# Kernel optimization log

Hardware: AMD Instinct MI355X
Metric: run time of the kernel (lower is better)

The kernel has to match this reference:

```python
import jax, jax.numpy as jnp
import numpy as np

EPS = 1e-5
K = 32          # nsample in PCT sample_and_group
S1, S2 = 512, 256


def _bn_relu(h, gamma, beta, axes):
    # BatchNorm1d in training mode: batch stats over (batch, length) per channel (last axis here)
    mu = jnp.mean(h, axes, keepdims=True)
    var = jnp.var(h, axes, keepdims=True)
    return jax.nn.relu((h - mu) * jax.lax.rsqrt(var + EPS) * gamma + beta)


def _index_points(points, idx):
    # points [B,N,C], idx [B,...] int -> [B,...,C]
    return jax.vmap(lambda p, i: p[i])(points, idx)


def _fps(xyz, npoint):
    # farthest point sampling; deterministic start at index 0. xyz [B,N,3] -> [B,npoint] int32
    B, N, _ = xyz.shape

    def body(carry, _):
        dmin, far = carry
        c = jnp.take_along_axis(xyz, far[:, None, None], axis=1)  # [B,1,3]
        dmin = jnp.minimum(dmin, jnp.sum((xyz - c) ** 2, -1))     # [B,N]
        return (dmin, jnp.argmax(dmin, -1).astype(jnp.int32)), far

    init = (jnp.full((B, N), 1e10, xyz.dtype), jnp.zeros((B,), jnp.int32))
    _, idxs = jax.lax.scan(body, init, None, length=npoint)
    return jnp.transpose(idxs)  # [B, npoint]


def _sg(features, xyz, s, w1, g1, b1, w2, g2, b2):
    # features [B,N,C], xyz [B,N,3] -> (new_xyz [B,s,3], out [B,s,out_ch])
    xyz_c = jax.lax.stop_gradient(xyz)
    fps_idx = _fps(xyz_c, s)                       # [B,s]
    new_xyz = _index_points(xyz, fps_idx)          # [B,s,3]
    new_pts = _index_points(features, fps_idx)     # [B,s,C]
    q = jax.lax.stop_gradient(new_xyz)
    # squared distances centers->all points, [B,s,N]
    d = (jnp.sum(q * q, -1)[:, :, None] + jnp.sum(xyz_c * xyz_c, -1)[:, None, :]
         - 2.0 * jnp.einsum('bsc,bnc->bsn', q, xyz_c))
    _, knn = jax.lax.top_k(-d, K)                  # [B,s,K] nearest neighbors
    grouped = _index_points(features, knn)         # [B,s,K,C]
    rel = grouped - new_pts[:, :, None, :]
    feat = jnp.concatenate([rel, jnp.broadcast_to(new_pts[:, :, None, :], rel.shape)], -1)  # [B,s,K,2C]
    h = _bn_relu(jnp.einsum('bskc,oc->bsko', feat, w1), g1, b1, (0, 1, 2))
    h = _bn_relu(jnp.einsum('bskc,oc->bsko', h, w2), g2, b2, (0, 1, 2))
    return new_xyz, jnp.max(h, axis=2)             # max over K neighbors -> [B,s,out]


def _forward(x, w1, g1, b1, w2, g2, b2,
             s1_w1, s1_g1, s1_b1, s1_w2, s1_g2, s1_b2,
             s2_w1, s2_g1, s2_b1, s2_w2, s2_g2, s2_b2):
    xyz = jnp.transpose(x, (0, 2, 1))                                # [B,N,3]
    f = _bn_relu(jnp.einsum('bcn,oc->bno', x, w1), g1, b1, (0, 1))   # [B,N,64]
    f = _bn_relu(jnp.einsum('bnc,oc->bno', f, w2), g2, b2, (0, 1))   # [B,N,64]
    xyz1, f1 = _sg(f, xyz, S1, s1_w1, s1_g1, s1_b1, s1_w2, s1_g2, s1_b2)   # [B,512,128]
    _, f2 = _sg(f1, xyz1, S2, s2_w1, s2_g1, s2_b1, s2_w2, s2_g2, s2_b2)    # [B,256,256]
    return jnp.transpose(f2, (0, 2, 1))                              # [B,256,256] channel-first


def setup_inputs() -> dict:
    key = jax.random.key(0)
    ks = jax.random.split(key, 8)
    B, N = 32, 4096
    inp = {"x": jax.random.normal(ks[0], (B, 3, N), jnp.float32)}

    def w(k, o, i):
        return jax.random.normal(k, (o, i), jnp.float32) * (1.0 / np.sqrt(i))

    inp["w1"] = w(ks[1], 64, 3);   inp["g1"] = jnp.ones((64,), jnp.float32);  inp["b1"] = jnp.zeros((64,), jnp.float32)
    inp["w2"] = w(ks[2], 64, 64);  inp["g2"] = jnp.ones((64,), jnp.float32);  inp["b2"] = jnp.zeros((64,), jnp.float32)
    inp["s1_w1"] = w(ks[3], 128, 128); inp["s1_g1"] = jnp.ones((128,), jnp.float32); inp["s1_b1"] = jnp.zeros((128,), jnp.float32)
    inp["s1_w2"] = w(ks[4], 128, 128); inp["s1_g2"] = jnp.ones((128,), jnp.float32); inp["s1_b2"] = jnp.zeros((128,), jnp.float32)
    inp["s2_w1"] = w(ks[5], 256, 256); inp["s2_g1"] = jnp.ones((256,), jnp.float32); inp["s2_b1"] = jnp.zeros((256,), jnp.float32)
    inp["s2_w2"] = w(ks[6], 256, 256); inp["s2_g2"] = jnp.ones((256,), jnp.float32); inp["s2_b2"] = jnp.zeros((256,), jnp.float32)
    return inp


def reference(x, w1, g1, b1, w2, g2, b2,
              s1_w1, s1_g1, s1_b1, s1_w2, s1_g2, s1_b2,
              s2_w1, s2_g1, s2_b1, s2_w2, s2_g2, s2_b2):
    return _forward(x, w1, g1, b1, w2, g2, b2,
                    s1_w1, s1_g1, s1_b1, s1_w2, s1_g2, s1_b2,
                    s2_w1, s2_g1, s2_b1, s2_w2, s2_g2, s2_b2)
```

## Files before the change

kernel.cpp:

```cpp
#include <hip/hip_runtime.h>

typedef short short8 __attribute__((ext_vector_type(8)));
typedef _Float16 h8 __attribute__((ext_vector_type(8)));
typedef float f32x4 __attribute__((ext_vector_type(4)));

#define DEVI __device__ __forceinline__

DEVI float h2f(short s) { return (float)__builtin_bit_cast(_Float16, s); }
DEVI short f2h(float f) { return __builtin_bit_cast(short, (_Float16)f); }
DEVI f32x4 mfma16(short8 a, short8 b, f32x4 c) {
  return __builtin_amdgcn_mfma_f32_16x16x32_f16(
      __builtin_bit_cast(h8, a), __builtin_bit_cast(h8, b), c, 0, 0, 0);
}

DEVI float wave_max_bcast(float v) {
  const int ID = 0xff800000;
  int x = __builtin_bit_cast(int, v);
#define STEPM(ctrl)                                                     \
  {                                                                     \
    int t = __builtin_amdgcn_update_dpp(ID, x, ctrl, 0xf, 0xf, false);  \
    x = __builtin_bit_cast(int, fmaxf(__builtin_bit_cast(float, x),     \
                                      __builtin_bit_cast(float, t)));   \
  }
  STEPM(0x111) STEPM(0x112) STEPM(0x114) STEPM(0x118) STEPM(0x142) STEPM(0x143)
#undef STEPM
  return __builtin_bit_cast(float, __builtin_amdgcn_readlane(x, 63));
}
DEVI float wave_min_bcast_f(float v) {
  const int ID = 0x7f800000;
  int x = __builtin_bit_cast(int, v);
#define STEPN(ctrl)                                                     \
  {                                                                     \
    int t = __builtin_amdgcn_update_dpp(ID, x, ctrl, 0xf, 0xf, false);  \
    x = __builtin_bit_cast(int, fminf(__builtin_bit_cast(float, x),     \
                                      __builtin_bit_cast(float, t)));   \
  }
  STEPN(0x111) STEPN(0x112) STEPN(0x114) STEPN(0x118) STEPN(0x142) STEPN(0x143)
#undef STEPN
  return __builtin_bit_cast(float, __builtin_amdgcn_readlane(x, 63));
}
DEVI unsigned wave_min_bcast_u(unsigned v) {
  const int ID = (int)0xffffffff;
  int x = (int)v;
#define STEPU(ctrl)                                                     \
  {                                                                     \
    int t = __builtin_amdgcn_update_dpp(ID, x, ctrl, 0xf, 0xf, false);  \
    x = (int)((unsigned)x < (unsigned)t ? (unsigned)x : (unsigned)t);   \
  }
  STEPU(0x111) STEPU(0x112) STEPU(0x114) STEPU(0x118) STEPU(0x142) STEPU(0x143)
#undef STEPU
  return (unsigned)__builtin_amdgcn_readlane(x, 63);
}
DEVI unsigned wave_iscan_add(unsigned v) {
  int x = (int)v, t;
  t = __builtin_amdgcn_update_dpp(0, x, 0x111, 0xf, 0xf, false); x += t;
  t = __builtin_amdgcn_update_dpp(0, x, 0x112, 0xf, 0xf, false); x += t;
  t = __builtin_amdgcn_update_dpp(0, x, 0x114, 0xf, 0xf, false); x += t;
  t = __builtin_amdgcn_update_dpp(0, x, 0x118, 0xf, 0xf, false); x += t;
  t = __builtin_amdgcn_update_dpp(0, x, 0x142, 0xa, 0xf, false); x += t;
  t = __builtin_amdgcn_update_dpp(0, x, 0x143, 0xc, 0xf, false); x += t;
  return (unsigned)x;
}

__global__ __launch_bounds__(256) void prep_kernel(
    const float* __restrict__ w2, const float* __restrict__ s1w2,
    const float* __restrict__ s2w2, const float* __restrict__ s1w1,
    const float* __restrict__ s2w1, short* __restrict__ w2b,
    short* __restrict__ s1w2b, short* __restrict__ s2w2b,
    short* __restrict__ W1pp, short* __restrict__ W2pp) {
  int i = blockIdx.x * 256 + threadIdx.x;
  if (i < 4096) {
    w2b[i] = f2h(w2[i]);
  } else if (i < 20480) {
    int j = i - 4096; s1w2b[j] = f2h(s1w2[j]);
  } else if (i < 86016) {
    int j = i - 20480; s2w2b[j] = f2h(s2w2[j]);
  } else if (i < 102400) {
    int j = i - 86016; int c = j & 127;
    float v = s1w1[j]; if (c >= 64) v -= s1w1[j - 64];
    W1pp[j] = f2h(v);
  } else if (i < 167936) {
    int j = i - 102400; int c = j & 255;
    float v = s2w1[j]; if (c >= 128) v -= s2w1[j - 128];
    W2pp[j] = f2h(v);
  }
}

__global__ __launch_bounds__(256) void stageA_kernel(
    const float* __restrict__ x, const float* __restrict__ w1,
    float* __restrict__ xyz, short* __restrict__ h0) {
  int i = blockIdx.x * 256 + threadIdx.x;
  int b = i >> 12, n = i & 4095;
  const float* xb = x + ((size_t)b * 3 << 12) + n;
  float x0 = xb[0], x1 = xb[4096], x2 = xb[8192];
  float* xp = xyz + (size_t)i * 3;
  xp[0] = x0; xp[1] = x1; xp[2] = x2;
  short* hp = h0 + ((size_t)i << 6);
#pragma unroll
  for (int o8 = 0; o8 < 8; ++o8) {
    short8 t;
#pragma unroll
    for (int j = 0; j < 8; ++j) {
      int o = o8 * 8 + j;
      float h = x0 * w1[o * 3] + x1 * w1[o * 3 + 1] + x2 * w1[o * 3 + 2];
      t[j] = f2h(h);
    }
    *reinterpret_cast<short8*>(hp + o8 * 8) = t;
  }
}


DEVI void stats64_body(int bid, int nb, int tid, const short* __restrict__ h,
                       float* __restrict__ partials, int M) {
  __shared__ float l0[256], l1[256];
  const int c = tid & 63, g = tid >> 6;
  float s0 = 0.f, s1 = 0.f;
  for (int m = bid * 4 + g; m < M; m += nb * 4) {
    float v = h2f(h[(size_t)m * 64 + c]);
    s0 += v; s1 += v * v;
  }
  l0[tid] = s0; l1[tid] = s1;
  __syncthreads();
  if (g == 0) {
    for (int w = 1; w < 4; ++w) { s0 += l0[c + w * 64]; s1 += l1[c + w * 64]; }
    partials[(size_t)c * nb + bid] = s0;
    partials[(size_t)(64 + c) * nb + bid] = s1;
  }
}

DEVI void reduce2_body(int c, int tid, const float* __restrict__ partials,
                       const float* __restrict__ gamma, const float* __restrict__ beta,
                       float* __restrict__ scale, float* __restrict__ shift,
                       int NB, int C, float invM) {
  __shared__ float l0[4], l1[4];
  const float* p0 = partials + (size_t)c * NB;
  const float* p1 = partials + (size_t)(C + c) * NB;
  float s0 = 0.f, s1 = 0.f;
  for (int i = tid; i < NB; i += 256) { s0 += p0[i]; s1 += p1[i]; }
#pragma unroll
  for (int off = 1; off < 64; off <<= 1) {
    s0 += __shfl_xor(s0, off);
    s1 += __shfl_xor(s1, off);
  }
  if ((tid & 63) == 0) { l0[tid >> 6] = s0; l1[tid >> 6] = s1; }
  __syncthreads();
  if (tid == 0) {
    s0 = l0[0] + l0[1] + l0[2] + l0[3];
    s1 = l1[0] + l1[1] + l1[2] + l1[3];
    float mean = s0 * invM;
    float var = fmaxf(s1 * invM - mean * mean, 0.f);
    float sc = gamma[c] / sqrtf(var + 1e-5f);
    scale[c] = sc;
    shift[c] = beta[c] - mean * sc;
  }
}

__global__ __launch_bounds__(256) void reduce2_kernel(
    const float* __restrict__ partials, const float* __restrict__ gamma,
    const float* __restrict__ beta, float* __restrict__ scale,
    float* __restrict__ shift, int NB, int C, float invM) {
  reduce2_body(blockIdx.x, threadIdx.x, partials, gamma, beta, scale, shift, NB, C, invM);
}

DEVI void apply_body(int bid, int tid, const short* __restrict__ h,
                     short* __restrict__ f, const float* __restrict__ scale,
                     const float* __restrict__ shift) {
  size_t i = ((size_t)bid * 256 + tid) * 8;
  int c0 = (int)(i & 63);
  short8 v = *reinterpret_cast<const short8*>(h + i);
  short8 o;
#pragma unroll
  for (int j = 0; j < 8; ++j) {
    float y = h2f(v[j]) * scale[c0 + j] + shift[c0 + j];
    o[j] = f2h(fmaxf(y, 0.f));
  }
  *reinterpret_cast<short8*>(f + i) = o;
}

template <int NPTS, int T>
DEVI void fps_seg_body(char* smemraw, int bid, int tid, const float* __restrict__ xyz,
                       int* __restrict__ out, float* __restrict__ xyzc, int nsel,
                       int it0, int it1, float* __restrict__ dming,
                       int* __restrict__ farg) {
  __builtin_amdgcn_s_setprio(1);
  constexpr int PT = NPTS / T;
  constexpr int NW = T / 64;
  float* sx = (float*)smemraw;
  float* sy = sx + NPTS;
  float* sz = sy + NPTS;
  float* wv = sz + NPTS;
  unsigned* wi = (unsigned*)(wv + 2 * NW);
  const int lane = tid & 63, wave = tid >> 6;
  const float* base = xyz + (size_t)bid * NPTS * 3;
  float px[PT], py[PT], pz[PT], dmin[PT];
#pragma unroll
  for (int j = 0; j < PT; ++j) {
    int n = j * T + tid;
    px[j] = base[n * 3]; py[j] = base[n * 3 + 1]; pz[j] = base[n * 3 + 2];
    sx[n] = px[j]; sy[n] = py[j]; sz[n] = pz[j];
  }
  int far;
  if (it0 == 0) {
#pragma unroll
    for (int j = 0; j < PT; ++j) dmin[j] = 1e10f;
    far = 0;
  } else {
#pragma unroll
    for (int j = 0; j < PT; ++j) dmin[j] = dming[(size_t)bid * NPTS + j * T + tid];
    far = farg[bid];
  }
  __syncthreads();
  float cx = sx[far], cy = sy[far], cz = sz[far];
  for (int it = it0; it < it1; ++it) {
    if (tid == 0) {
      out[bid * nsel + it] = far;
      if (xyzc) {
        float* xc = xyzc + ((size_t)bid * nsel + it) * 3;
        xc[0] = cx; xc[1] = cy; xc[2] = cz;
      }
    }
    float bv = -1.f;
#pragma unroll
    for (int j = 0; j < PT; ++j) {
      float dx = __fsub_rn(px[j], cx), dy = __fsub_rn(py[j], cy), dz = __fsub_rn(pz[j], cz);
      float d = __fadd_rn(__fadd_rn(__fmul_rn(dx, dx), __fmul_rn(dy, dy)), __fmul_rn(dz, dz));
      float dm = fminf(dmin[j], d);
      dmin[j] = dm;
      bv = fmaxf(bv, dm);
    }
    float wmv = wave_max_bcast(bv);
    unsigned ci = 0xffffffffu;
#pragma unroll
    for (int j = PT - 1; j >= 0; --j)
      if (dmin[j] == wmv) ci = (unsigned)(j * T + tid);
    unsigned wmi = wave_min_bcast_u(ci);
    const int bsel = it & 1;
    if (lane == 0) { wv[bsel * NW + wave] = wmv; wi[bsel * NW + wave] = wmi; }
    __syncthreads();
    const int e = lane & (NW - 1);
    float v = wv[bsel * NW + e];
    unsigned si = wi[bsel * NW + e];
#define CMB(ctrl)                                                                        \
  {                                                                                      \
    float v2 = __builtin_bit_cast(                                                       \
        float, __builtin_amdgcn_update_dpp(0, __builtin_bit_cast(int, v), ctrl, 0xf, 0xf, true)); \
    unsigned i2 = (unsigned)__builtin_amdgcn_update_dpp(0, (int)si, ctrl, 0xf, 0xf, true);\
    bool bt = (v2 > v) || (v2 == v && i2 < si);                                          \
    v = bt ? v2 : v; si = bt ? i2 : si;                                                  \
  }
    if constexpr (NW >= 2) CMB(0x121)
    if constexpr (NW >= 4) CMB(0x122)
    if constexpr (NW >= 8) CMB(0x124)
#undef CMB
    far = (int)si;
    cx = sx[far]; cy = sy[far]; cz = sz[far];
  }
  if (it1 < nsel) {
#pragma unroll
    for (int j = 0; j < PT; ++j) dming[(size_t)bid * NPTS + j * T + tid] = dmin[j];
    if (tid == 0) farg[bid] = far;
  }
}

#define KNN_SMEM_BYTES ((4096 + 256 + 4 + 256 + 256) * 4)
template <int NPTS, int S>
DEVI void knn_body(char* smemraw, int bs, int tid, const float* __restrict__ pts,
                   const int* __restrict__ fpsidx, int* __restrict__ knn) {
  constexpr int PT = NPTS / 256;
  unsigned* hist = (unsigned*)smemraw;
  unsigned* csums = hist + 4096;
  unsigned* meta = csums + 256;
  float* bval = (float*)(meta + 4);
  unsigned* bidx = (unsigned*)(bval + 256);
  const int lane = tid & 63, wave = tid >> 6;
  const int b = bs / S;
  const int cidx = fpsidx[bs];
  const float* cp = pts + ((size_t)b * NPTS + cidx) * 3;
  const float qx = cp[0], qy = cp[1], qz = cp[2];
  const float qq = __fadd_rn(__fadd_rn(__fmul_rn(qx, qx), __fmul_rn(qy, qy)), __fmul_rn(qz, qz));
  const float* base = pts + (size_t)b * NPTS * 3;
  float d[PT]; unsigned u[PT];
#pragma unroll
  for (int j = 0; j < PT; ++j) {
    int n = j * 256 + tid;
    float x = base[n * 3], y = base[n * 3 + 1], z = base[n * 3 + 2];
    float pp = __fadd_rn(__fadd_rn(__fmul_rn(x, x), __fmul_rn(y, y)), __fmul_rn(z, z));
    float dot = __fadd_rn(__fadd_rn(__fmul_rn(qx, x), __fmul_rn(qy, y)), __fmul_rn(qz, z));
    d[j] = __fsub_rn(__fadd_rn(qq, pp), __fmul_rn(2.f, dot));
    unsigned bits = __builtin_bit_cast(unsigned, d[j]);
    unsigned m = (unsigned)((int)bits >> 31);
    u[j] = bits ^ (m | 0x80000000u);
  }
  {
    uint4 z4 = {0u, 0u, 0u, 0u};
    uint4* hq = (uint4*)hist;
    for (int i = tid; i < 1024; i += 256) hq[i] = z4;
    if (tid == 0) { meta[0] = 0; meta[3] = 0; }
  }
  __syncthreads();
#pragma unroll
  for (int j = 0; j < PT; ++j) atomicAdd(&hist[u[j] >> 20], 1u);
  __syncthreads();
  {
    const uint4* hq = (const uint4*)(hist + tid * 16);
    unsigned cs = 0;
#pragma unroll
    for (int q = 0; q < 4; ++q) {
      uint4 v = hq[q];
      cs += v.x + v.y + v.z + v.w;
    }
    csums[tid] = cs;
  }
  __syncthreads();
  if (wave == 0) {
    const int t4 = lane * 4;
    unsigned c0 = csums[t4], c1 = csums[t4 + 1], c2 = csums[t4 + 2], c3 = csums[t4 + 3];
    unsigned lt = c0 + c1 + c2 + c3;
    unsigned incl = wave_iscan_add(lt);
    unsigned excl = incl - lt;
    unsigned long long blt = __ballot(incl >= 32u);
    int L = __ffsll((long long)blt) - 1;
    if (lane == L) {
      unsigned cum = excl;
      int bucket = -1;
      unsigned cc[4] = {c0, c1, c2, c3};
#pragma unroll
      for (int q = 0; q < 4; ++q) {
        if (bucket < 0 && cum + cc[q] >= 32u) {
          int bbase = (t4 + q) * 16;
          for (int h = 0; h < 16; ++h) {
            unsigned hv = hist[bbase + h];
            if (cum + hv >= 32u) { bucket = bbase + h; break; }
            cum += hv;
          }
        } else if (bucket < 0) {
          cum += cc[q];
        }
      }
      meta[1] = (unsigned)bucket;
      meta[2] = cum;
    }
  }
  __syncthreads();
  const unsigned B = meta[1];
  const unsigned cb = meta[2];
  int* kout = knn + (size_t)bs * 32;
#pragma unroll
  for (int j = 0; j < PT; ++j) {
    unsigned bk = u[j] >> 20;
    if (bk < B) {
      unsigned p = atomicAdd(&meta[0], 1u);
      kout[p] = j * 256 + tid;
    } else if (bk == B) {
      unsigned p = atomicAdd(&meta[3], 1u);
      if (p < 256u) { bval[p] = d[j]; bidx[p] = (unsigned)(j * 256 + tid); }
    }
  }
  __syncthreads();
  const int m = 32 - (int)cb;
  if (wave == 0 && m > 0) {
    unsigned nb = meta[3]; if (nb > 256u) nb = 256u;
    float v0 = (lane < (int)nb) ? bval[lane] : 3.4e38f;
    unsigned i0 = (lane < (int)nb) ? bidx[lane] : 0xffffffffu;
    float v1 = (lane + 64 < (int)nb) ? bval[lane + 64] : 3.4e38f;
    unsigned i1 = (lane + 64 < (int)nb) ? bidx[lane + 64] : 0xffffffffu;
    float v2 = (lane + 128 < (int)nb) ? bval[lane + 128] : 3.4e38f;
    unsigned i2 = (lane + 128 < (int)nb) ? bidx[lane + 128] : 0xffffffffu;
    float v3 = (lane + 192 < (int)nb) ? bval[lane + 192] : 3.4e38f;
    unsigned i3 = (lane + 192 < (int)nb) ? bidx[lane + 192] : 0xffffffffu;
    for (int k = 0; k < m; ++k) {
      float lv = v0; unsigned li = i0;
      if (v1 < lv || (v1 == lv && i1 < li)) { lv = v1; li = i1; }
      if (v2 < lv || (v2 == lv && i2 < li)) { lv = v2; li = i2; }
      if (v3 < lv || (v3 == lv && i3 < li)) { lv = v3; li = i3; }
      float wmv = wave_min_bcast_f(lv);
      unsigned ci = (lv == wmv) ? li : 0xffffffffu;
      unsigned wmi = wave_min_bcast_u(ci);
      if (lane == 0) kout[cb + k] = (int)wmi;
      if (i0 == wmi) { v0 = 3.4e38f; i0 = 0xffffffffu; }
      if (i1 == wmi) { v1 = 3.4e38f; i1 = 0xffffffffu; }
      if (i2 == wmi) { v2 = 3.4e38f; i2 = 0xffffffffu; }
      if (i3 == wmi) { v3 = 3.4e38f; i3 = 0xffffffffu; }
    }
  }
}

template <int KD, int ND, bool GATHER, bool BNA, int NPTS, int S, int EPI>
DEVI void gemm_body(char* smemraw, int bid, int tid, int gemmBlocks,
                    const short* A, const int* KNNp, const int* FPSp,
                    const short* __restrict__ W, const float* __restrict__ bnscale,
                    const float* __restrict__ bnshift, short* Hout,
                    float* __restrict__ mmax, float* __restrict__ mmin,
                    float* __restrict__ partials) {
  constexpr int C = KD / 2;
  constexpr int NT = (ND > 128) ? 8 : ND / 16;
  constexpr int BR = (ND > 128) ? 64 : 128;
  constexpr int KC = (ND >= 256) ? 64 : KD;
  constexpr int LOG2KC = (KC == 64) ? 6 : 7;
  constexpr int NCH = KD / KC;
  constexpr int KTC = KC / 32;
  constexpr int LROW = KC + 8;
  constexpr int TROW = ND + 8;
  constexpr int LBB = ND * LROW * 2;
  constexpr int TBB = BR * TROW * 2;
  constexpr int LSOFF = (LBB > TBB) ? LBB : TBB;
  short* lb = (short*)smemraw;
  float* lstats = (float*)(smemraw + LSOFF);
  const int wave = tid >> 6, lane = tid & 63;
  const int rowOff = (ND > 128) ? (wave >> 1) * 32 : wave * 32;
  const int colOff = (ND > 128) ? (wave & 1) * 128 : 0;
  const int mBase = bid * BR + rowOff;
  for (int i = tid; i < 2 * ND; i += 256) lstats[i] = 0.f;

  const short* aptr[2][2];
#pragma unroll
  for (int rg = 0; rg < 2; ++rg) {
    int m = mBase + rg * 16 + (lane & 15);
    if constexpr (GATHER) {
      int idx = KNNp[m];
      int bb = m / (S * 32);
      int s = (m - bb * (S * 32)) >> 5;
      int fidx = FPSp[bb * S + s];
      aptr[rg][0] = A + ((size_t)bb * NPTS + idx) * C;
      aptr[rg][1] = A + ((size_t)bb * NPTS + fidx) * C;
    } else {
      aptr[rg][0] = A + (size_t)m * KD;
      aptr[rg][1] = A + (size_t)m * KD + C;
    }
  }
  const int koLane = (lane >> 4) * 8;
  f32x4 acc[2][NT];
#pragma unroll
  for (int rg = 0; rg < 2; ++rg)
#pragma unroll
    for (int nt = 0; nt < NT; ++nt) acc[rg][nt] = (f32x4){0.f, 0.f, 0.f, 0.f};

#pragma unroll
  for (int ch = 0; ch < NCH; ++ch) {
    __syncthreads();
    constexpr int SIT = (ND * KC) / 2048;
#pragma unroll
    for (int i = 0; i < SIT; ++i) {
      int e = i * 2048 + tid * 8;
      int n = e >> LOG2KC, kk = e & (KC - 1);
      short8 v = *reinterpret_cast<const short8*>(W + (size_t)n * KD + ch * KC + kk);
      *reinterpret_cast<short8*>(&lb[n * LROW + kk]) = v;
    }
    __syncthreads();
#pragma unroll
    for (int ktc = 0; ktc < KTC; ++ktc) {
      const int kt = ch * KTC + ktc;
      const int half = (kt * 32 >= C) ? 1 : 0;
      const int ko = kt * 32 + koLane;
      const int koh = ko - half * C;
      short8 afrag[2];
#pragma unroll
      for (int rg = 0; rg < 2; ++rg) {
        short8 a = *reinterpret_cast<const short8*>(aptr[rg][half] + koh);
        if constexpr (BNA) {
          const float* scp = bnscale + ko;
          const float* shp = bnshift + ko;
#pragma unroll
          for (int j = 0; j < 8; ++j) {
            float v = h2f(a[j]);
            v = fmaxf(v * scp[j] + shp[j], 0.f);
            a[j] = f2h(v);
          }
        }
        afrag[rg] = a;
      }
#pragma unroll
      for (int nt = 0; nt < NT; ++nt) {
        short8 bfr = *reinterpret_cast<const short8*>(
            &lb[(colOff + nt * 16 + (lane & 15)) * LROW + ktc * 32 + koLane]);
        acc[0][nt] = mfma16(afrag[0], bfr, acc[0][nt]);
        acc[1][nt] = mfma16(afrag[1], bfr, acc[1][nt]);
      }
    }
  }
  __syncthreads();

#pragma unroll
  for (int nt = 0; nt < NT; ++nt) {
    float s0 = 0.f, s1 = 0.f;
#pragma unroll
    for (int rg = 0; rg < 2; ++rg)
#pragma unroll
      for (int i = 0; i < 4; ++i) {
        float v = acc[rg][nt][i];
        s0 += v; s1 += v * v;
      }
    s0 += __shfl_xor(s0, 16); s0 += __shfl_xor(s0, 32);
    s1 += __shfl_xor(s1, 16); s1 += __shfl_xor(s1, 32);
    if (lane < 16) {
      atomicAdd(&lstats[colOff + nt * 16 + lane], s0);
      atomicAdd(&lstats[ND + colOff + nt * 16 + lane], s1);
    }
  }

  if constexpr (EPI == 0) {
#pragma unroll
    for (int rg = 0; rg < 2; ++rg)
#pragma unroll
      for (int nt = 0; nt < NT; ++nt)
#pragma unroll
        for (int i = 0; i < 4; ++i) {
          int r = rowOff + rg * 16 + (lane >> 4) * 4 + i;
          int n = colOff + nt * 16 + (lane & 15);
          lb[r * TROW + n] = f2h(acc[rg][nt][i]);
        }
    __syncthreads();
    constexpr int TPR = ND / 8;
    constexpr int RPI = 256 / TPR;
    const int r0 = tid / TPR, c0 = (tid % TPR) * 8;
#pragma unroll
    for (int it = 0; it < BR / RPI; ++it) {
      int r = it * RPI + r0;
      short8 v = *reinterpret_cast<const short8*>(&lb[r * TROW + c0]);
      *reinterpret_cast<short8*>(&Hout[(size_t)(bid * BR + r) * ND + c0]) = v;
    }
  } else {
    const int center = (bid * BR + rowOff) >> 5;
#pragma unroll
    for (int nt = 0; nt < NT; ++nt) {
      float mx = -3.4e38f, mn = 3.4e38f;
#pragma unroll
      for (int rg = 0; rg < 2; ++rg)
#pragma unroll
        for (int i = 0; i < 4; ++i) {
          float v = acc[rg][nt][i];
          mx = fmaxf(mx, v); mn = fminf(mn, v);
        }
      mx = fmaxf(mx, __shfl_xor(mx, 16)); mx = fmaxf(mx, __shfl_xor(mx, 32));
      mn = fminf(mn, __shfl_xor(mn, 16)); mn = fminf(mn, __shfl_xor(mn, 32));
      if (lane < 16) {
        mmax[(size_t)center * ND + colOff + nt * 16 + lane] = mx;
        mmin[(size_t)center * ND + colOff + nt * 16 + lane] = mn;
      }
    }
    __syncthreads();
  }
  for (int i = tid; i < 2 * ND; i += 256)
    partials[(size_t)i * gemmBlocks + bid] = lstats[i];
}


template <int FN, int FT>
__global__ __launch_bounds__(256, 1) void fps_stats_seg(
    int fpsBlocks, const float* fxyz, int* fout, float* fxyzc, int fnsel,
    int it0, int it1, float* dming, int* farg,
    const short* sh, float* sp, int sM, int snb) {
  extern __shared__ char smem[];
  if ((int)blockIdx.x < fpsBlocks)
    fps_seg_body<FN, FT>(smem, blockIdx.x, threadIdx.x, fxyz, fout, fxyzc, fnsel,
                         it0, it1, dming, farg);
  else
    stats64_body(blockIdx.x - fpsBlocks, snb, threadIdx.x, sh, sp, sM);
}

template <int FN, int FT, int KNPTS, int KS>
__global__ __launch_bounds__(256, 1) void fps_r2_knn_seg(
    int fpsBlocks, int compBlocks, const float* fxyz, int* fout, float* fxyzc,
    int fnsel, int it0, int it1, float* dming, int* farg,
    const float* partials, const float* gamma, const float* beta,
    float* scale, float* shift, int NB, int C, float invM,
    const float* kpts, const int* kfps, int* kout, int ks0) {
  extern __shared__ char smem[];
  const int bx = (int)blockIdx.x;
  if (bx < fpsBlocks) {
    fps_seg_body<FN, FT>(smem, bx, threadIdx.x, fxyz, fout, fxyzc, fnsel,
                         it0, it1, dming, farg);
  } else if (bx < fpsBlocks + compBlocks) {
    reduce2_body(bx - fpsBlocks, threadIdx.x, partials, gamma, beta, scale,
                 shift, NB, C, invM);
  } else {
    int kb = bx - fpsBlocks - compBlocks;
    int bs = (kb >> 7) * KS + ks0 + (kb & 127);
    knn_body<KNPTS, KS>(smem, bs, threadIdx.x, kpts, kfps, kout);
  }
}

template <int FN, int FT, int KD, int ND, bool BNA, int EPI, int KNPTS, int KS>
__global__ __launch_bounds__(256, 1) void fps_gemm_knn_seg(
    int fpsBlocks, int compBlocks, const float* fxyz, int* fout, float* fxyzc,
    int fnsel, int it0, int it1, float* dming, int* farg,
    const short* A, const short* W, const float* bnscale, const float* bnshift,
    short* Hout, float* partials,
    const float* kpts, const int* kfps, int* kout, int ks0) {
  extern __shared__ char smem[];
  const int bx = (int)blockIdx.x;
  if (bx < fpsBlocks) {
    fps_seg_body<FN, FT>(smem, bx, threadIdx.x, fxyz, fout, fxyzc, fnsel,
                         it0, it1, dming, farg);
  } else if (bx < fpsBlocks + compBlocks) {
    gemm_body<KD, ND, false, BNA, 1, 1, EPI>(smem, bx - fpsBlocks, threadIdx.x,
                                             compBlocks, A, nullptr, nullptr,
                                             W, bnscale, bnshift, Hout, nullptr,
                                             nullptr, partials);
  } else {
    int kb = bx - fpsBlocks - compBlocks;
    int bs = (kb >> 7) * KS + ks0 + (kb & 127);
    knn_body<KNPTS, KS>(smem, bs, threadIdx.x, kpts, kfps, kout);
  }
}

template <int F2N, int NPTS, int S>
__global__ __launch_bounds__(256, 4) void fps2_knn_apply_kernel(
    int f2Blocks, const float* f2xyz, int* f2out, int f2nsel, int it0, int it1,
    float* dming2, int* farg2,
    int knnBlocks, const float* kpts, const int* kfps, int* kout, int ks0,
    const short* ah, short* af, const float* ascale, const float* ashift) {
  __shared__ __align__(16) char smem[KNN_SMEM_BYTES];
  const int bx = (int)blockIdx.x;
  if (bx < f2Blocks) {
    fps_seg_body<F2N, 256>(smem, bx, threadIdx.x, f2xyz, f2out, nullptr, f2nsel,
                           it0, it1, dming2, farg2);
  } else if (bx < f2Blocks + knnBlocks) {
    int kb = bx - f2Blocks;
    int bs = (kb >> 7) * S + ks0 + (kb & 127);
    knn_body<NPTS, S>(smem, bs, threadIdx.x, kpts, kfps, kout);
  } else {
    apply_body(bx - f2Blocks - knnBlocks, threadIdx.x, ah, af, ascale, ashift);
  }
}

template <int F2N, int KD, int ND, int NPTS, int S>
__global__ __launch_bounds__(256, 4) void mega1_kernel(
    int f2Blocks, const float* f2xyz, int* f2out, int f2nsel, int it0, int it1,
    float* dming2, int* farg2,
    const short* A, const int* KNNp, const int* FPSp, const short* W,
    short* Hout, float* partials) {
  extern __shared__ char smem[];
  const int bx = (int)blockIdx.x;
  if (bx < f2Blocks) {
    fps_seg_body<F2N, 256>(smem, bx, threadIdx.x, f2xyz, f2out, nullptr, f2nsel,
                           it0, it1, dming2, farg2);
  } else {
    int gb = bx - f2Blocks;
    const int gB = (int)gridDim.x - f2Blocks;
    const int q = gB >> 3;
    gb = (gb & 7) * q + (gb >> 3);
    gemm_body<KD, ND, true, false, NPTS, S, 0>(smem, gb, threadIdx.x, gB, A, KNNp,
                                               FPSp, W, nullptr, nullptr, Hout,
                                               nullptr, nullptr, partials);
  }
}

template <int F2N, int KD, int ND>
__global__ __launch_bounds__(256, 4) void fps2_gemm_kernel(
    int f2Blocks, const float* f2xyz, int* f2out, int f2nsel, int it0, int it1,
    float* dming2, int* farg2,
    const short* A, const short* W, const float* bnscale, const float* bnshift,
    float* mmax, float* mmin, float* partials) {
  extern __shared__ char smem[];
  const int bx = (int)blockIdx.x;
  if (bx < f2Blocks) {
    fps_seg_body<F2N, 256>(smem, bx, threadIdx.x, f2xyz, f2out, nullptr, f2nsel,
                           it0, it1, dming2, farg2);
  } else {
    gemm_body<KD, ND, false, true, 1, 1, 1>(smem, bx - f2Blocks, threadIdx.x,
                                            (int)gridDim.x - f2Blocks, A, nullptr,
                                            nullptr, W, bnscale, bnshift, nullptr,
                                            mmax, mmin, partials);
  }
}

template <int KD, int ND, bool GATHER, bool BNA, int NPTS, int S, int EPI>
__global__ __launch_bounds__(256, 4) void gemm_kernel(
    const short* A, const int* KNNp, const int* FPSp, const short* W,
    const float* bnscale, const float* bnshift, short* Hout,
    float* mmax, float* mmin, float* partials) {
  extern __shared__ char smem[];
  int bid = (int)blockIdx.x;
  if constexpr (GATHER) {
    const int q = (int)gridDim.x >> 3;
    bid = (bid & 7) * q + (bid >> 3);
  }
  gemm_body<KD, ND, GATHER, BNA, NPTS, S, EPI>(smem, bid, threadIdx.x,
                                               gridDim.x, A, KNNp, FPSp, W, bnscale,
                                               bnshift, Hout, mmax, mmin, partials);
}

template <int NPTS, int S>
__global__ __launch_bounds__(256, 4) void maxpool_knn_kernel(
    int knnBlocks, const float* pts, const int* fpsidx, int* knn,
    const float* mmax, const float* mmin, const float* scale, const float* shift,
    short* f1) {
  __shared__ __align__(16) char smem[KNN_SMEM_BYTES];
  if ((int)blockIdx.x < knnBlocks) {
    knn_body<NPTS, S>(smem, blockIdx.x, threadIdx.x, pts, fpsidx, knn);
  } else {
    const int ctr = (blockIdx.x - knnBlocks) * 2 + (threadIdx.x >> 7);
    const int c = threadIdx.x & 127;
    const float sc = scale[c], sh = shift[c];
    float y = (sc >= 0.f) ? mmax[(size_t)ctr * 128 + c] : mmin[(size_t)ctr * 128 + c];
    f1[(size_t)ctr * 128 + c] = f2h(fmaxf(sc * y + sh, 0.f));
  }
}

__global__ __launch_bounds__(256) void maxpool_out_kernel(
    const float* __restrict__ mmax, const float* __restrict__ mmin,
    const float* __restrict__ scale, const float* __restrict__ shift,
    float* __restrict__ out) {
  const int bs = blockIdx.x, c = threadIdx.x;
  const int b = bs >> 8, s = bs & 255;
  const float sc = scale[c], sh = shift[c];
  float y = (sc >= 0.f) ? mmax[(size_t)bs * 256 + c] : mmin[(size_t)bs * 256 + c];
  out[((size_t)b << 16) + ((size_t)c << 8) + s] = fmaxf(sc * y + sh, 0.f);
}

extern "C" void kernel_launch(void* const* d_in, const int* in_sizes, int n_in,
                              void* d_out, int out_size, void* d_ws, size_t ws_size,
                              hipStream_t stream) {
  (void)in_sizes; (void)n_in; (void)out_size; (void)ws_size;
  const float* x    = (const float*)d_in[0];
  const float* w1   = (const float*)d_in[1];
  const float* g1   = (const float*)d_in[2];
  const float* b1   = (const float*)d_in[3];
  const float* w2   = (const float*)d_in[4];
  const float* g2   = (const float*)d_in[5];
  const float* b2   = (const float*)d_in[6];
  const float* s1w1 = (const float*)d_in[7];
  const float* s1g1 = (const float*)d_in[8];
  const float* s1b1 = (const float*)d_in[9];
  const float* s1w2 = (const float*)d_in[10];
  const float* s1g2 = (const float*)d_in[11];
  const float* s1b2 = (const float*)d_in[12];
  const float* s2w1 = (const float*)d_in[13];
  const float* s2g1 = (const float*)d_in[14];
  const float* s2b1 = (const float*)d_in[15];
  const float* s2w2 = (const float*)d_in[16];
  const float* s2g2 = (const float*)d_in[17];
  const float* s2b2 = (const float*)d_in[18];
  float* out = (float*)d_out;

  char* ws = (char*)d_ws;
  size_t off = 0;
  auto alloc = [&](size_t bytes) -> char* {
    size_t p = (off + 255) & ~(size_t)255;
    off = p + bytes;
    return ws + p;
  };

  float* xyz      = (float*)alloc(32ull * 4096 * 3 * 4);
  short* h0       = (short*)alloc(32ull * 4096 * 64 * 2);
  short* hb       = (short*)alloc(32ull * 4096 * 64 * 2);
  short* fb       = (short*)alloc(32ull * 4096 * 64 * 2);
  int*   fps1     = (int*)alloc(32ull * 512 * 4);
  float* xyzc1    = (float*)alloc(32ull * 512 * 3 * 4);
  int*   knn1     = (int*)alloc(32ull * 512 * 32 * 4);
  short* f1       = (short*)alloc(32ull * 512 * 128 * 2);
  int*   fps2     = (int*)alloc(32ull * 256 * 4);
  int*   knn2     = (int*)alloc(32ull * 256 * 32 * 4);
  float* dming    = (float*)alloc(32ull * 4096 * 4);
  int*   farg     = (int*)alloc(32 * 4);
  float* dming2   = (float*)alloc(32ull * 512 * 4);
  int*   farg2    = (int*)alloc(32 * 4);
  short* hbuf     = (short*)alloc(134217728ull);
  float* mm1max   = (float*)alloc(16384ull * 128 * 4);
  float* mm1min   = (float*)alloc(16384ull * 128 * 4);
  float* mm2max   = (float*)alloc(8192ull * 256 * 4);
  float* mm2min   = (float*)alloc(8192ull * 256 * 4);
  float* partials = (float*)alloc(2ull * 256 * 4096 * 4);
  float* scA  = (float*)alloc(64 * 4);  float* shA  = (float*)alloc(64 * 4);
  float* scBc = (float*)alloc(64 * 4);  float* shBc = (float*)alloc(64 * 4);
  float* sc1a = (float*)alloc(128 * 4); float* sh1a = (float*)alloc(128 * 4);
  float* sc1b = (float*)alloc(128 * 4); float* sh1b = (float*)alloc(128 * 4);
  float* sc2a = (float*)alloc(256 * 4); float* sh2a = (float*)alloc(256 * 4);
  float* sc2b = (float*)alloc(256 * 4); float* sh2b = (float*)alloc(256 * 4);
  short* w2b   = (short*)alloc(4096 * 2);
  short* s1w2b = (short*)alloc(16384 * 2);
  short* s2w2b = (short*)alloc(65536 * 2);
  short* W1pp  = (short*)alloc(16384 * 2);
  short* W2pp  = (short*)alloc(65536 * 2);

  prep_kernel<<<656, 256, 0, stream>>>(w2, s1w2, s2w2, s1w1, s2w1, w2b, s1w2b, s2w2b, W1pp, W2pp);
  stageA_kernel<<<512, 256, 0, stream>>>(x, w1, xyz, h0);

  fps_stats_seg<4096, 256><<<288, 256, 49216, stream>>>(
      32, xyz, fps1, xyzc1, 512, 0, 128, dming, farg, h0, partials, 131072, 256);
  fps_r2_knn_seg<4096, 256, 4096, 512><<<4192, 256, 49216, stream>>>(
      32, 64, xyz, fps1, xyzc1, 512, 128, 256, dming, farg,
      partials, g1, b1, scA, shA, 256, 64, 1.f / 131072.f,
      xyz, fps1, knn1, 0);
  fps_gemm_knn_seg<4096, 256, 64, 64, true, 0, 4096, 512><<<5152, 256, 49216, stream>>>(
      32, 1024, xyz, fps1, xyzc1, 512, 256, 384, dming, farg,
      h0, w2b, scA, shA, hb, partials,
      xyz, fps1, knn1, 128);
  fps_r2_knn_seg<4096, 256, 4096, 512><<<4192, 256, 49216, stream>>>(
      32, 64, xyz, fps1, xyzc1, 512, 384, 512, dming, farg,
      partials, g2, b2, scBc, shBc, 1024, 64, 1.f / 131072.f,
      xyz, fps1, knn1, 256);

  fps2_knn_apply_kernel<512, 4096, 512><<<8224, 256, 0, stream>>>(
      32, xyzc1, fps2, 256, 0, 86, dming2, farg2,
      4096, xyz, fps1, knn1, 384, hb, fb, scBc, shBc);

  mega1_kernel<512, 128, 128, 4096, 512><<<4128, 256, 35840, stream>>>(
      32, xyzc1, fps2, 256, 86, 171, dming2, farg2,
      fb, knn1, fps1, W1pp, hbuf, partials);
  reduce2_kernel<<<128, 256, 0, stream>>>(partials, s1g1, s1b1, sc1a, sh1a, 4096, 128, 1.f / 524288.f);

  fps2_gemm_kernel<512, 128, 128><<<4128, 256, 35840, stream>>>(
      32, xyzc1, fps2, 256, 171, 256, dming2, farg2,
      hbuf, s1w2b, sc1a, sh1a, mm1max, mm1min, partials);
  reduce2_kernel<<<128, 256, 0, stream>>>(partials, s1g2, s1b2, sc1b, sh1b, 4096, 128, 1.f / 524288.f);

  maxpool_knn_kernel<512, 256><<<16384, 256, 0, stream>>>(
      8192, xyzc1, fps2, knn2, mm1max, mm1min, sc1b, sh1b, f1);

  gemm_kernel<256, 256, true, false, 512, 256, 0><<<4096, 256, 38912, stream>>>(
      f1, knn2, fps2, W2pp, nullptr, nullptr, hbuf, nullptr, nullptr, partials);
  reduce2_kernel<<<256, 256, 0, stream>>>(partials, s2g1, s2b1, sc2a, sh2a, 4096, 256, 1.f / 262144.f);
  gemm_kernel<256, 256, false, true, 1, 1, 1><<<4096, 256, 38912, stream>>>(
      hbuf, nullptr, nullptr, s2w2b, sc2a, sh2a, nullptr, mm2max, mm2min, partials);
  reduce2_kernel<<<256, 256, 0, stream>>>(partials, s2g2, s2b2, sc2b, sh2b, 4096, 256, 1.f / 262144.f);
  maxpool_out_kernel<<<8192, 256, 0, stream>>>(mm2max, mm2min, sc2b, sh2b, out);
}
```

Before: 795.2 us.

## Fold BN-apply into stage-1 gather GEMM and overlap it with KNN blocks

Removes the standalone BN+ReLU apply pass that wrote a normalized copy of the stage-0 features. The stage-1 gather GEMM now reads the raw features and applies scale/shift on load, using a duplicated 128-wide scale/shift table for the concatenated rel/center channels. Most GEMM blocks are moved into the FPS2/KNN kernel so they co-run with the remaining KNN work, and the rest stay in mega1. This saves a full read/write pass over the feature buffer, but every gathered neighbor now repeats the affine work, and correctness depends on KNN rows for each GEMM block being finished before that block runs.

```diff
diff --git a/kernel.cpp b/kernel.cpp
--- a/kernel.cpp
+++ b/kernel.cpp
@@ -131,7 +131,7 @@
 DEVI void reduce2_body(int c, int tid, const float* __restrict__ partials,
                        const float* __restrict__ gamma, const float* __restrict__ beta,
                        float* __restrict__ scale, float* __restrict__ shift,
-                       int NB, int C, float invM) {
+                       int NB, int C, float invM, int dupC) {
   __shared__ float l0[4], l1[4];
   const float* p0 = partials + (size_t)c * NB;
   const float* p1 = partials + (size_t)(C + c) * NB;
@@ -150,8 +150,10 @@
     float mean = s0 * invM;
     float var = fmaxf(s1 * invM - mean * mean, 0.f);
     float sc = gamma[c] / sqrtf(var + 1e-5f);
+    float sh = beta[c] - mean * sc;
     scale[c] = sc;
-    shift[c] = beta[c] - mean * sc;
+    shift[c] = sh;
+    if (dupC) { scale[c + C] = sc; shift[c + C] = sh; }
   }
 }
 
@@ -159,22 +161,8 @@
     const float* __restrict__ partials, const float* __restrict__ gamma,
     const float* __restrict__ beta, float* __restrict__ scale,
     float* __restrict__ shift, int NB, int C, float invM) {
-  reduce2_body(blockIdx.x, threadIdx.x, partials, gamma, beta, scale, shift, NB, C, invM);
-}
-
-DEVI void apply_body(int bid, int tid, const short* __restrict__ h,
-                     short* __restrict__ f, const float* __restrict__ scale,
-                     const float* __restrict__ shift) {
-  size_t i = ((size_t)bid * 256 + tid) * 8;
-  int c0 = (int)(i & 63);
-  short8 v = *reinterpret_cast<const short8*>(h + i);
-  short8 o;
-#pragma unroll
-  for (int j = 0; j < 8; ++j) {
-    float y = h2f(v[j]) * scale[c0 + j] + shift[c0 + j];
-    o[j] = f2h(fmaxf(y, 0.f));
-  }
-  *reinterpret_cast<short8*>(f + i) = o;
+  reduce2_body(blockIdx.x, threadIdx.x, partials, gamma, beta, scale, shift, NB, C,
+               invM, 0);
 }
 
 template <int NPTS, int T>
@@ -563,7 +551,7 @@
     int fpsBlocks, int compBlocks, const float* fxyz, int* fout, float* fxyzc,
     int fnsel, int it0, int it1, float* dming, int* farg,
     const float* partials, const float* gamma, const float* beta,
-    float* scale, float* shift, int NB, int C, float invM,
+    float* scale, float* shift, int NB, int C, float invM, int dupC,
     const float* kpts, const int* kfps, int* kout, int ks0) {
   extern __shared__ char smem[];
   const int bx = (int)blockIdx.x;
@@ -572,7 +560,7 @@
                          it0, it1, dming, farg);
   } else if (bx < fpsBlocks + compBlocks) {
     reduce2_body(bx - fpsBlocks, threadIdx.x, partials, gamma, beta, scale,
-                 shift, NB, C, invM);
+                 shift, NB, C, invM, dupC);
   } else {
     int kb = bx - fpsBlocks - compBlocks;
     int bs = (kb >> 7) * KS + ks0 + (kb & 127);
@@ -604,32 +592,43 @@
   }
 }
 
-template <int F2N, int NPTS, int S>
-__global__ __launch_bounds__(256, 4) void fps2_knn_apply_kernel(
+template <int F2N, int KNPTS, int KS, int KD, int ND, int NPTS, int S,
+          int JCNT, int JOFF, int BPB>
+__global__ __launch_bounds__(256, 4) void fps2_knn_gemm_kernel(
     int f2Blocks, const float* f2xyz, int* f2out, int f2nsel, int it0, int it1,
     float* dming2, int* farg2,
     int knnBlocks, const float* kpts, const int* kfps, int* kout, int ks0,
-    const short* ah, short* af, const float* ascale, const float* ashift) {
-  __shared__ __align__(16) char smem[KNN_SMEM_BYTES];
+    const short* A, const int* KNNp, const int* FPSp, const short* W,
+    const float* bnscale, const float* bnshift, short* Hout, float* partials,
+    int gemmTotal) {
+  extern __shared__ char smem[];
   const int bx = (int)blockIdx.x;
   if (bx < f2Blocks) {
     fps_seg_body<F2N, 256>(smem, bx, threadIdx.x, f2xyz, f2out, nullptr, f2nsel,
                            it0, it1, dming2, farg2);
   } else if (bx < f2Blocks + knnBlocks) {
     int kb = bx - f2Blocks;
-    int bs = (kb >> 7) * S + ks0 + (kb & 127);
-    knn_body<NPTS, S>(smem, bs, threadIdx.x, kpts, kfps, kout);
+    int bs = (kb >> 7) * KS + ks0 + (kb & 127);
+    knn_body<KNPTS, KS>(smem, bs, threadIdx.x, kpts, kfps, kout);
   } else {
-    apply_body(bx - f2Blocks - knnBlocks, threadIdx.x, ah, af, ascale, ashift);
-  }
-}
-
-template <int F2N, int KD, int ND, int NPTS, int S>
+    int gb = bx - f2Blocks - knnBlocks;
+    const int gB = (int)gridDim.x - f2Blocks - knnBlocks;
+    const int q = gB >> 3;
+    gb = (gb & 7) * q + (gb >> 3);
+    int bid = (gb / JCNT) * BPB + JOFF + (gb % JCNT);
+    gemm_body<KD, ND, true, true, NPTS, S, 0>(smem, bid, threadIdx.x, gemmTotal,
+                                              A, KNNp, FPSp, W, bnscale, bnshift,
+                                              Hout, nullptr, nullptr, partials);
+  }
+}
+
+template <int F2N, int KD, int ND, int NPTS, int S, int JCNT, int JOFF, int BPB>
 __global__ __launch_bounds__(256, 4) void mega1_kernel(
     int f2Blocks, const float* f2xyz, int* f2out, int f2nsel, int it0, int it1,
     float* dming2, int* farg2,
     const short* A, const int* KNNp, const int* FPSp, const short* W,
-    short* Hout, float* partials) {
+    const float* bnscale, const float* bnshift, short* Hout, float* partials,
+    int gemmTotal) {
   extern __shared__ char smem[];
   const int bx = (int)blockIdx.x;
   if (bx < f2Blocks) {
@@ -640,9 +639,11 @@
     const int gB = (int)gridDim.x - f2Blocks;
     const int q = gB >> 3;
     gb = (gb & 7) * q + (gb >> 3);
-    gemm_body<KD, ND, true, false, NPTS, S, 0>(smem, gb, threadIdx.x, gB, A, KNNp,
-                                               FPSp, W, nullptr, nullptr, Hout,
-                                               nullptr, nullptr, partials);
+    int bid = (gb / JCNT) * BPB + JOFF + (gb % JCNT);
+    gemm_body<KD, ND, true, true, NPTS, S, 0>(smem, bid, threadIdx.x,
+                                              gemmTotal, A, KNNp, FPSp, W, bnscale,
+                                              bnshift, Hout, nullptr, nullptr,
+                                              partials);
   }
 }
 
@@ -745,7 +746,6 @@
   float* xyz      = (float*)alloc(32ull * 4096 * 3 * 4);
   short* h0       = (short*)alloc(32ull * 4096 * 64 * 2);
   short* hb       = (short*)alloc(32ull * 4096 * 64 * 2);
-  short* fb       = (short*)alloc(32ull * 4096 * 64 * 2);
   int*   fps1     = (int*)alloc(32ull * 512 * 4);
   float* xyzc1    = (float*)alloc(32ull * 512 * 3 * 4);
   int*   knn1     = (int*)alloc(32ull * 512 * 32 * 4);
@@ -762,12 +762,12 @@
   float* mm2max   = (float*)alloc(8192ull * 256 * 4);
   float* mm2min   = (float*)alloc(8192ull * 256 * 4);
   float* partials = (float*)alloc(2ull * 256 * 4096 * 4);
-  float* scA  = (float*)alloc(64 * 4);  float* shA  = (float*)alloc(64 * 4);
-  float* scBc = (float*)alloc(64 * 4);  float* shBc = (float*)alloc(64 * 4);
-  float* sc1a = (float*)alloc(128 * 4); float* sh1a = (float*)alloc(128 * 4);
-  float* sc1b = (float*)alloc(128 * 4); float* sh1b = (float*)alloc(128 * 4);
-  float* sc2a = (float*)alloc(256 * 4); float* sh2a = (float*)alloc(256 * 4);
-  float* sc2b = (float*)alloc(256 * 4); float* sh2b = (float*)alloc(256 * 4);
+  float* scA  = (float*)alloc(64 * 4);   float* shA  = (float*)alloc(64 * 4);
+  float* scBcD = (float*)alloc(128 * 4); float* shBcD = (float*)alloc(128 * 4);
+  float* sc1a = (float*)alloc(128 * 4);  float* sh1a = (float*)alloc(128 * 4);
+  float* sc1b = (float*)alloc(128 * 4);  float* sh1b = (float*)alloc(128 * 4);
+  float* sc2a = (float*)alloc(256 * 4);  float* sh2a = (float*)alloc(256 * 4);
+  float* sc2b = (float*)alloc(256 * 4);  float* sh2b = (float*)alloc(256 * 4);
   short* w2b   = (short*)alloc(4096 * 2);
   short* s1w2b = (short*)alloc(16384 * 2);
   short* s2w2b = (short*)alloc(65536 * 2);
@@ -781,7 +781,7 @@
       32, xyz, fps1, xyzc1, 512, 0, 128, dming, farg, h0, partials, 131072, 256);
   fps_r2_knn_seg<4096, 256, 4096, 512><<<4192, 256, 49216, stream>>>(
       32, 64, xyz, fps1, xyzc1, 512, 128, 256, dming, farg,
-      partials, g1, b1, scA, shA, 256, 64, 1.f / 131072.f,
+      partials, g1, b1, scA, shA, 256, 64, 1.f / 131072.f, 0,
       xyz, fps1, knn1, 0);
   fps_gemm_knn_seg<4096, 256, 64, 64, true, 0, 4096, 512><<<5152, 256, 49216, stream>>>(
       32, 1024, xyz, fps1, xyzc1, 512, 256, 384, dming, farg,
@@ -789,16 +789,18 @@
       xyz, fps1, knn1, 128);
   fps_r2_knn_seg<4096, 256, 4096, 512><<<4192, 256, 49216, stream>>>(
       32, 64, xyz, fps1, xyzc1, 512, 384, 512, dming, farg,
-      partials, g2, b2, scBc, shBc, 1024, 64, 1.f / 131072.f,
+      partials, g2, b2, scBcD, shBcD, 1024, 64, 1.f / 131072.f, 1,
       xyz, fps1, knn1, 256);
 
-  fps2_knn_apply_kernel<512, 4096, 512><<<8224, 256, 0, stream>>>(
+  fps2_knn_gemm_kernel<512, 4096, 512, 128, 128, 4096, 512, 96, 0, 128>
+      <<<7200, 256, 35840, stream>>>(
       32, xyzc1, fps2, 256, 0, 86, dming2, farg2,
-      4096, xyz, fps1, knn1, 384, hb, fb, scBc, shBc);
-
-  mega1_kernel<512, 128, 128, 4096, 512><<<4128, 256, 35840, stream>>>(
+      4096, xyz, fps1, knn1, 384,
+      hb, knn1, fps1, W1pp, scBcD, shBcD, hbuf, partials, 4096);
+
+  mega1_kernel<512, 128, 128, 4096, 512, 32, 96, 128><<<1056, 256, 35840, stream>>>(
       32, xyzc1, fps2, 256, 86, 171, dming2, farg2,
-      fb, knn1, fps1, W1pp, hbuf, partials);
+      hb, knn1, fps1, W1pp, scBcD, shBcD, hbuf, partials, 4096);
   reduce2_kernel<<<128, 256, 0, stream>>>(partials, s1g1, s1b1, sc1a, sh1a, 4096, 128, 1.f / 524288.f);
 
   fps2_gemm_kernel<512, 128, 128><<<4128, 256, 35840, stream>>>(
```

Result: slower. 820.5 us (+3.2%).
